# Performance work log

Hardware: AMD Instinct MI355X
Metric: run time of the kernel (lower is better)

## Reference

```python
import jax, jax.numpy as jnp
import numpy as np
import math

C = 96; HEADS = 3; HD = C // HEADS; WS = 8; B = 4; H = 256; W = 256
EPS = 1e-5; SCALE = HD ** -0.5; LOGIT_MAX = math.log(1.0 / 0.01)
N = WS * WS


def _rel_pos():
    coords = np.stack(np.meshgrid(np.arange(WS), np.arange(WS), indexing='ij')).reshape(2, -1)
    rel = (coords[:, :, None] - coords[:, None, :]).transpose(1, 2, 0).astype(np.float32)
    return jnp.asarray(np.sign(rel) * np.log1p(np.abs(rel)))  # [N, N, 2]

REL = _rel_pos()


def conv1x1(x, w, b):
    return jnp.einsum('bchw,oc->bohw', x, w) + b[None, :, None, None]


def dwconv(x, w, b, pad, reflect=False):
    if reflect:
        x = jnp.pad(x, ((0, 0), (0, 0), (pad, pad), (pad, pad)), mode='reflect')
        padding = 'VALID'
    else:
        padding = [(pad, pad), (pad, pad)]
    y = jax.lax.conv_general_dilated(x, w, (1, 1), padding,
                                     feature_group_count=x.shape[1],
                                     dimension_numbers=('NCHW', 'OIHW', 'NCHW'))
    return y + b[None, :, None, None]


def window_partition(x):  # [B,H,W,C] -> [nW, WS*WS, C]
    b, h, w, c = x.shape
    x = x.reshape(b, h // WS, WS, w // WS, WS, c).transpose(0, 1, 3, 2, 4, 5)
    return x.reshape(-1, WS * WS, c)


def window_reverse(win, h, w):  # [nW, WS*WS, C] -> [B,H,W,C]
    b = win.shape[0] // ((h // WS) * (w // WS))
    x = win.reshape(b, h // WS, w // WS, WS, WS, -1).transpose(0, 1, 3, 2, 4, 5)
    return x.reshape(b, h, w, -1)


def setup_inputs() -> dict:
    key = jax.random.key(0)
    ks = jax.random.split(key, 16)
    def nrm(k, shape, std=0.02):
        return jax.random.normal(k, shape, jnp.float32) * std
    inp = {'x': jax.random.normal(ks[0], (B, C, H, W), jnp.float32)}
    inp.update(
        agn_weight=jnp.ones((C,), jnp.float32), agn_bias=jnp.zeros((C,), jnp.float32),
        meta1_w=nrm(ks[1], (C,)), meta1_b=jnp.ones((C,), jnp.float32),
        meta2_w=nrm(ks[2], (C,)), meta2_b=jnp.zeros((C,), jnp.float32),
        la1_w=nrm(ks[3], (C, 1, 3, 3)), la1_b=jnp.zeros((C,), jnp.float32),
        la2_w=nrm(ks[4], (C, 1, 3, 3)), la2_b=jnp.zeros((C,), jnp.float32),
        ta1_w=nrm(ks[5], (C, 1, 3, 3)), ta1_b=jnp.zeros((C,), jnp.float32),
        ta2_w=nrm(ks[6], (C, 1, 3, 3)), ta2_b=jnp.zeros((C,), jnp.float32),
        q_w=nrm(ks[7], (C, C)), q_b=jnp.zeros((C,), jnp.float32),
        kv_w=nrm(ks[8], (2 * C, C)), kv_b=jnp.zeros((2 * C,), jnp.float32),
        dw_w=nrm(ks[9], (C, 1, 5, 5)), dw_b=jnp.zeros((C,), jnp.float32),
        proj_w=nrm(ks[10], (C, C)), proj_b=jnp.zeros((C,), jnp.float32),
        logit_scale=jnp.asarray(math.log(1.0 / 0.07), jnp.float32),
        rp_w1=nrm(ks[11], (256, 2)), rp_b1=jnp.zeros((256,), jnp.float32),
        rp_w2=nrm(ks[12], (HEADS, 256)), rp_b2=jnp.zeros((HEADS,), jnp.float32),
        m1_w=nrm(ks[13], (4 * C, C)), m1_b=jnp.zeros((4 * C,), jnp.float32),
        m2_w=nrm(ks[14], (C, 4 * C)), m2_b=jnp.zeros((C,), jnp.float32),
    )
    return inp


def reference(x, agn_weight, agn_bias, meta1_w, meta1_b, meta2_w, meta2_b,
              la1_w, la1_b, la2_w, la2_b, ta1_w, ta1_b, ta2_w, ta2_b,
              q_w, q_b, kv_w, kv_b, dw_w, dw_b, proj_w, proj_b,
              logit_scale, rp_w1, rp_b1, rp_w2, rp_b2,
              m1_w, m1_b, m2_w, m2_b):
    identity = x
    # ---- AGN: per-sample global mean/std norm + dynamic affine + two dw-conv branches
    mean = jnp.mean(x, axis=(1, 2, 3), keepdims=True)                      # [B,1,1,1]
    std = jnp.sqrt(jnp.mean((x - mean) ** 2, axis=(1, 2, 3), keepdims=True) + EPS)
    xn = (x - mean) / std
    rescale = std * meta1_w[None, :, None, None] + meta1_b[None, :, None, None]   # conv1x1(1->C) on std
    rebias = mean * meta2_w[None, :, None, None] + meta2_b[None, :, None, None]
    local = dwconv(jax.nn.relu(dwconv(xn, la1_w, la1_b, 1)), la2_w, la2_b, 1)
    texture = dwconv(jax.nn.relu(dwconv(xn, ta1_w, ta1_b, 1)), ta2_w, ta2_b, 1)
    xn = xn * (agn_weight[None, :, None, None] * rescale) + (agn_bias[None, :, None, None] + rebias) + local + texture
    # ---- DSAttention (use_attn, DWConv, shift_size=0, H%WS==0 so no padding)
    Q = conv1x1(xn, q_w, q_b)
    KV = conv1x1(xn, kv_w, kv_b)                                           # [B,2C,H,W]
    qkv_img = jnp.concatenate([Q, KV], axis=1).transpose(0, 2, 3, 1)       # [B,H,W,3C]
    co = dwconv(Q, dw_w, dw_b, 2, reflect=True).transpose(0, 2, 3, 1)      # reflect-padded 5x5 dwconv
    qkv = window_partition(qkv_img)                                        # [nW,N,3C]
    cw = window_partition(co)                                              # [nW,N,C]
    nW = qkv.shape[0]
    qkv = qkv.reshape(nW, N, 3, HEADS, HD).transpose(2, 0, 3, 1, 4)        # [3,nW,h,N,hd]
    q = cw.reshape(nW, N, HEADS, HD).transpose(0, 2, 1, 3)                 # q replaced by conv branch
    k = qkv[1] * SCALE
    v = qkv[2]
    ls = jnp.exp(jnp.minimum(logit_scale, LOGIT_MAX))
    hb = jax.nn.relu(REL @ rp_w1.T + rp_b1)                                # [N,N,256]
    bias = (hb @ rp_w2.T + rp_b2).transpose(2, 0, 1)                       # [h,N,N]
    attn = jax.nn.softmax(jnp.einsum('whnd,whmd->whnm', q, k) * ls + bias[None], axis=-1)
    o = jnp.einsum('whnm,whmd->whnd', attn, v).transpose(0, 2, 1, 3).reshape(nW, N, C)
    out = window_reverse(o, x.shape[2], x.shape[3]).transpose(0, 3, 1, 2)  # [B,C,H,W]
    a = conv1x1(out, proj_w, proj_b)
    x = identity + a * rescale + rebias
    # ---- MLP (1x1 conv -> ReLU -> 1x1 conv), residual
    x = x + conv1x1(jax.nn.relu(conv1x1(x, m1_w, m1_b)), m2_w, m2_b)
    return x
```

## Files before the change

### kernel.cpp

```cpp
#include <hip/hip_runtime.h>
#include <hip/hip_bf16.h>

typedef __hip_bfloat16 bf16;

#define PER_B     6291456
#define EPS_F     1e-5f
#define SCALE_F   0.17677669529663687f
#define LOGIT_MAX_F 4.605170185988092f

__device__ __forceinline__ float b2f(bf16 v){ return __bfloat162float(v); }
__device__ __forceinline__ bf16  f2b(float v){ return __float2bfloat16(v); }

template<int DT> __device__ __forceinline__ float rdf(const void* p, size_t i){
  return DT ? ((const float*)p)[i] : b2f(((const bf16*)p)[i]);
}
template<int DT> __device__ __forceinline__ void wrf(void* p, size_t i, float v){
  if (DT) ((float*)p)[i] = v; else ((bf16*)p)[i] = f2b(v);
}
template<int DT> __device__ __forceinline__ float2 rd2(const void* p, size_t i){
  if (DT) return *(const float2*)((const float*)p + i);
  unsigned u = *(const unsigned*)((const bf16*)p + i);
  return make_float2(__uint_as_float(u << 16), __uint_as_float(u & 0xffff0000u));
}

typedef __attribute__((ext_vector_type(8))) short short8v;
typedef __attribute__((ext_vector_type(4))) short short4v;
typedef __attribute__((ext_vector_type(4))) float f32x4;

__device__ __forceinline__ short f2bs(float v){
  unsigned u = __float_as_uint(v);
  return (short)((u + 0x7fffu + ((u >> 16) & 1u)) >> 16);
}
__device__ __forceinline__ float bs2f(short s){
  return __uint_as_float(((unsigned)(unsigned short)s) << 16);
}

template<int DT> __device__ __forceinline__ short8v ld8(const void* p, size_t i){
  short8v a;
  if (DT){
    const float* f = (const float*)p + i;
    float4 lo = *(const float4*)f;
    float4 hi = *(const float4*)(f + 4);
    a[0]=f2bs(lo.x); a[1]=f2bs(lo.y); a[2]=f2bs(lo.z); a[3]=f2bs(lo.w);
    a[4]=f2bs(hi.x); a[5]=f2bs(hi.y); a[6]=f2bs(hi.z); a[7]=f2bs(hi.w);
  } else {
    a = *(const short8v*)((const short*)p + i);
  }
  return a;
}
template<int DT> __device__ __forceinline__ short8v ld4x2(const void* p, size_t i0){
  short8v a;
  if (DT){
    const float* f = (const float*)p;
    float4 lo = *(const float4*)(f + i0);
    float4 hi = *(const float4*)(f + i0 + 16);
    a[0]=f2bs(lo.x); a[1]=f2bs(lo.y); a[2]=f2bs(lo.z); a[3]=f2bs(lo.w);
    a[4]=f2bs(hi.x); a[5]=f2bs(hi.y); a[6]=f2bs(hi.z); a[7]=f2bs(hi.w);
  } else {
    const short* s = (const short*)p;
    short4v lo = *(const short4v*)(s + i0);
    short4v hi = *(const short4v*)(s + i0 + 16);
    a[0]=lo[0]; a[1]=lo[1]; a[2]=lo[2]; a[3]=lo[3];
    a[4]=hi[0]; a[5]=hi[1]; a[6]=hi[2]; a[7]=hi[3];
  }
  return a;
}

__global__ __launch_bounds__(256) void k_detect(const void* __restrict__ x, int* __restrict__ flag){
  __shared__ int cnt;
  if (threadIdx.x == 0) cnt = 0;
  __syncthreads();
  float v = b2f(((const bf16*)x)[(size_t)threadIdx.x * 16]);
  int bad = (!(v == v)) || (fabsf(v) > 1e20f);
  if (bad) atomicAdd(&cnt, 1);
  __syncthreads();
  if (threadIdx.x == 0) *flag = (cnt >= 4) ? 1 : 0;
}

template<int DT>
__global__ __launch_bounds__(256) void k_stats_partial(const void* __restrict__ x,
    float* __restrict__ partials, const int* __restrict__ flag){
  if (*flag != DT) return;
  int blk = blockIdx.x;
  int b = blk >> 8, chunk = blk & 255;
  const int chunkN = PER_B / 256;
  size_t base = (size_t)b * PER_B + (size_t)chunk * chunkN;
  float s = 0.f, ss = 0.f;
  if (DT){
    const float4* p4 = (const float4*)((const float*)x + base);
    for (int i = threadIdx.x; i < chunkN/4; i += 256){
      float4 v = p4[i];
      s  += v.x + v.y + v.z + v.w;
      ss += v.x*v.x + v.y*v.y + v.z*v.z + v.w*v.w;
    }
  } else {
    const short8v* p8 = (const short8v*)((const short*)x + base);
    for (int i = threadIdx.x; i < chunkN/8; i += 256){
      short8v v = p8[i];
      #pragma unroll
      for (int k = 0; k < 8; k++){
        float f = bs2f(v[k]); s += f; ss += f*f;
      }
    }
  }
  __shared__ float sh[512];
  sh[threadIdx.x] = s; sh[256 + threadIdx.x] = ss;
  __syncthreads();
  for (int st = 128; st > 0; st >>= 1){
    if (threadIdx.x < st){
      sh[threadIdx.x]     += sh[threadIdx.x + st];
      sh[256+threadIdx.x] += sh[256+threadIdx.x + st];
    }
    __syncthreads();
  }
  if (threadIdx.x == 0){ partials[blk*2] = sh[0]; partials[blk*2+1] = sh[256]; }
}

template<int DT>
__global__ __launch_bounds__(256) void k_stats_final(const float* __restrict__ partials,
    const void* m1w, const void* m1b, const void* m2w, const void* m2b,
    float* __restrict__ stats, const int* __restrict__ flag){
  if (*flag != DT) return;
  __shared__ float sh[512];
  __shared__ float mS[4], sS[4];
  for (int b = 0; b < 4; b++){
    sh[threadIdx.x]     = partials[(b*256+threadIdx.x)*2];
    sh[256+threadIdx.x] = partials[(b*256+threadIdx.x)*2+1];
    __syncthreads();
    for (int st = 128; st > 0; st >>= 1){
      if (threadIdx.x < st){
        sh[threadIdx.x]     += sh[threadIdx.x + st];
        sh[256+threadIdx.x] += sh[256+threadIdx.x + st];
      }
      __syncthreads();
    }
    if (threadIdx.x == 0){
      float mean = sh[0] / (float)PER_B;
      float var  = sh[256] / (float)PER_B - mean*mean;
      float stdv = sqrtf(var + EPS_F);
      mS[b] = mean; sS[b] = stdv;
      stats[b] = mean; stats[4+b] = stdv;
    }
    __syncthreads();
  }
  for (int t = threadIdx.x; t < 384; t += 256){
    int b = t / 96, c = t % 96;
    stats[8+t]   = sS[b]*rdf<DT>(m1w,c) + rdf<DT>(m1b,c);
    stats[392+t] = mS[b]*rdf<DT>(m2w,c) + rdf<DT>(m2b,c);
  }
}

template<int DT>
__global__ __launch_bounds__(256) void k_bias(const void* w1, const void* b1v,
    const void* w2, const void* b2v, float* __restrict__ biasT, const int* __restrict__ flag){
  if (*flag != DT) return;
  int i = blockIdx.x >> 6, j = blockIdx.x & 63;
  int dy = (i>>3) - (j>>3), dx = (i&7) - (j&7);
  float fy = (float)dy, fx = (float)dx;
  float r0 = copysignf(log1pf(fabsf(fy)), fy);
  float r1 = copysignf(log1pf(fabsf(fx)), fx);
  int t = threadIdx.x;
  float hb = fmaxf(r0*rdf<DT>(w1,t*2) + r1*rdf<DT>(w1,t*2+1) + rdf<DT>(b1v,t), 0.f);
  __shared__ float sh[256];
  for (int h = 0; h < 3; h++){
    sh[t] = hb * rdf<DT>(w2, h*256+t);
    __syncthreads();
    for (int st = 128; st > 0; st >>= 1){ if (t < st) sh[t] += sh[t+st]; __syncthreads(); }
    if (t == 0) biasT[h*4096 + j*64 + i] = sh[0] + rdf<DT>(b2v, h);
    __syncthreads();
  }
}

template<int DT>
__global__ __launch_bounds__(256) void k_agn_fused(const void* __restrict__ x,
    const float* __restrict__ stats,
    const void* la1w, const void* la1b, const void* la2w, const void* la2b,
    const void* ta1w, const void* ta1b, const void* ta2w, const void* ta2b,
    const void* agnw, const void* agnb,
    bf16* __restrict__ xn2, const int* __restrict__ flag){
  if (*flag != DT) return;
  __shared__ float xs[1296];
  __shared__ float ts[1156];
  __shared__ float us[1156];
  int idx = blockIdx.x;
  int tile = idx & 63; int bc = idx >> 6; int c = bc % 96; int b = bc / 96;
  int oy = (tile >> 3) << 5, ox = (tile & 7) << 5;
  float mean = stats[b], sd = stats[4+b];
  size_t xbase = ((size_t)bc) << 16;
  for (int it = threadIdx.x; it < 1296; it += 256){
    int ly = it / 36, lx = it % 36;
    int gy = oy - 2 + ly, gx = ox - 2 + lx;
    float v = 0.f;
    if (gy >= 0 && gy < 256 && gx >= 0 && gx < 256)
      v = (rdf<DT>(x, xbase + (gy<<8) + gx) - mean) / sd;
    xs[it] = v;
  }
  float wl1[9], wt1[9], wl2[9], wt2[9];
  #pragma unroll
  for (int k = 0; k < 9; k++){
    wl1[k] = rdf<DT>(la1w, c*9+k); wt1[k] = rdf<DT>(ta1w, c*9+k);
    wl2[k] = rdf<DT>(la2w, c*9+k); wt2[k] = rdf<DT>(ta2w, c*9+k);
  }
  float bl1 = rdf<DT>(la1b, c), bt1 = rdf<DT>(ta1b, c);
  __syncthreads();
  for (int it = threadIdx.x; it < 1156; it += 256){
    int ly = it / 34, lx = it % 34;
    int cy = oy - 1 + ly, cx = ox - 1 + lx;
    float a1 = 0.f, a2 = 0.f;
    if (cy >= 0 && cy < 256 && cx >= 0 && cx < 256){
      a1 = bl1; a2 = bt1;
      #pragma unroll
      for (int dy = 0; dy < 3; dy++)
        #pragma unroll
        for (int dx = 0; dx < 3; dx++){
          float v = xs[(ly+dy)*36 + lx+dx];
          a1 += v * wl1[dy*3+dx]; a2 += v * wt1[dy*3+dx];
        }
      a1 = fmaxf(a1, 0.f); a2 = fmaxf(a2, 0.f);
    }
    ts[it] = a1; us[it] = a2;
  }
  __syncthreads();
  float agw = rdf<DT>(agnw,c)*stats[8+bc];
  float agb = rdf<DT>(agnb,c) + stats[392+bc];
  float bl2 = rdf<DT>(la2b, c), bt2 = rdf<DT>(ta2b, c);
  #pragma unroll
  for (int k = 0; k < 4; k++){
    int px = threadIdx.x + (k << 8);
    int ly = px >> 5, lx = px & 31;
    float l = bl2, t = bt2;
    #pragma unroll
    for (int dy = 0; dy < 3; dy++)
      #pragma unroll
      for (int dx = 0; dx < 3; dx++){
        l += ts[(ly+dy)*34 + lx+dx] * wl2[dy*3+dx];
        t += us[(ly+dy)*34 + lx+dx] * wt2[dy*3+dx];
      }
    float v = xs[(ly+2)*36 + lx+2];
    float r = v*agw + agb + l + t;
    xn2[xbase + ((oy+ly)<<8) + ox + lx] = f2b(r);
  }
}

#define CS_OFF 0
#define XS_OFF 13312
#define QB_OFF 43264
#define KT_OFF 13312
#define VD_OFF 26624
#define XC_OFF 40448
#define PS_OFF 40448
#define OS_OFF 13312

template<int DT>
__global__ __launch_bounds__(256, 3) void k_attn_mega(const bf16* __restrict__ xn2,
    const void* qw, const void* qb, const void* kvw, const void* kvb,
    const void* dww, const void* dwb, const void* pw, const void* pb,
    const void* lsin, const float* __restrict__ biasT,
    const void* __restrict__ xin, const float* __restrict__ stats,
    void* __restrict__ outp, const int* __restrict__ flag){
  if (*flag != DT) return;
  __shared__ __align__(16) char smem[53760];
  int tid = threadIdx.x, wid = blockIdx.x;
  int b = wid >> 10, wy = (wid >> 5) & 31, wx = wid & 31;
  int wv = tid >> 6, ln = tid & 63;
  int r = ln & 15, q = ln >> 4;

  {
    short* xs = (short*)(smem + XS_OFF);
    for (int it = tid; it < 13824; it += 256){
      int t = it % 144, craw = it / 144;
      int c = craw ^ ((t >> 3) & 7);
      int ty = (wy<<3) - 2 + t/12, tx = (wx<<3) - 2 + t%12;
      ty = ty < 0 ? -ty : (ty > 255 ? 510 - ty : ty);
      tx = tx < 0 ? -tx : (tx > 255 ? 510 - tx : tx);
      xs[t*104 + c] = ((const short*)xn2)[(((size_t)(b*96 + c))<<16) + (ty<<8) + tx];
    }
  }
  __syncthreads();

  {
    const short* xs = (const short*)(smem + XS_OFF);
    short* Qb = (short*)(smem + QB_OFF) + wv*1184;
    short* cs = (short*)(smem + CS_OFF);
    int ty0 = (ln>>3)+2, tx0 = (ln&7)+2;
    for (int mt = wv; mt < 6; mt += 4){
      short8v aw[3];
      #pragma unroll
      for (int kt = 0; kt < 3; kt++)
        aw[kt] = ld8<DT>(qw, (size_t)(16*mt + r)*96 + 32*kt + 8*q);
      float qb4[4];
      #pragma unroll
      for (int j = 0; j < 4; j++) qb4[j] = rdf<DT>(qb, 16*mt + 4*q + j);
      float accs[9][4];
      #pragma unroll
      for (int nt = 0; nt < 9; nt++){
        f32x4 acc = {0.f,0.f,0.f,0.f};
        #pragma unroll
        for (int kt = 0; kt < 3; kt++){
          short8v bx = *(const short8v*)(xs + (16*nt + r)*104 + 32*kt + 8*q);
          acc = __builtin_amdgcn_mfma_f32_16x16x32_bf16(aw[kt], bx, acc, 0, 0, 0);
        }
        #pragma unroll
        for (int j = 0; j < 4; j++) accs[nt][j] = acc[j] + qb4[j];
      }
      if (q < 2){
        #pragma unroll
        for (int nt = 0; nt < 9; nt++)
          #pragma unroll
          for (int j = 0; j < 4; j++)
            Qb[(4*q+j)*148 + 16*nt + r] = f2bs(accs[nt][j]);
      }
      asm volatile("s_waitcnt lgkmcnt(0)" ::: "memory");
      for (int cl = 0; cl < 8; cl++){
        int c = 16*mt + cl;
        float a = rdf<DT>(dwb, c);
        #pragma unroll
        for (int dy = -2; dy <= 2; dy++)
          #pragma unroll
          for (int dx = -2; dx <= 2; dx++)
            a += bs2f(Qb[cl*148 + (ty0+dy)*12 + tx0+dx]) * rdf<DT>(dww, c*25 + (dy+2)*5 + dx+2);
        cs[ln*104 + c] = f2bs(a);
      }
      asm volatile("s_waitcnt lgkmcnt(0)" ::: "memory");
      if (q >= 2){
        #pragma unroll
        for (int nt = 0; nt < 9; nt++)
          #pragma unroll
          for (int j = 0; j < 4; j++)
            Qb[(4*(q-2)+j)*148 + 16*nt + r] = f2bs(accs[nt][j]);
      }
      asm volatile("s_waitcnt lgkmcnt(0)" ::: "memory");
      for (int cl = 8; cl < 16; cl++){
        int c = 16*mt + cl;
        float a = rdf<DT>(dwb, c);
        #pragma unroll
        for (int dy = -2; dy <= 2; dy++)
          #pragma unroll
          for (int dx = -2; dx <= 2; dx++)
            a += bs2f(Qb[(cl-8)*148 + (ty0+dy)*12 + tx0+dx]) * rdf<DT>(dww, c*25 + (dy+2)*5 + dx+2);
        cs[ln*104 + c] = f2bs(a);
      }
      asm volatile("s_waitcnt lgkmcnt(0)" ::: "memory");
    }
  }
  __syncthreads();

  {
    short* xc = (short*)(smem + XC_OFF);
    for (int it = tid; it < 768; it += 256){
      int c = it >> 3, row = it & 7;
      const short* src = (const short*)xn2 + (((size_t)(b*96 + c))<<16)
                         + (((wy<<3)+row)<<8) + (wx<<3);
      short8v v = *(const short8v*)src;
      #pragma unroll
      for (int k = 0; k < 8; k++){
        int pe = k ^ row;
        xc[(row*8+pe)*104 + c] = v[pe];
      }
    }
  }
  __syncthreads();
  {
    const short* xc = (const short*)(smem + XC_OFF);
    short* Kt = (short*)(smem + KT_OFF);
    short* Vd = (short*)(smem + VD_OFF);
    for (int mtk = wv; mtk < 12; mtk += 4){
      short8v aw[3];
      #pragma unroll
      for (int kt = 0; kt < 3; kt++)
        aw[kt] = ld8<DT>(kvw, (size_t)(16*mtk + r)*96 + 32*kt + 8*q);
      float bb[4];
      #pragma unroll
      for (int j = 0; j < 4; j++) bb[j] = rdf<DT>(kvb, 16*mtk + 4*q + j);
      for (int nt = 0; nt < 4; nt++){
        f32x4 acc = {0.f,0.f,0.f,0.f};
        #pragma unroll
        for (int kt = 0; kt < 3; kt++){
          short8v bx = *(const short8v*)(xc + (16*nt + r)*104 + 32*kt + 8*q);
          acc = __builtin_amdgcn_mfma_f32_16x16x32_bf16(aw[kt], bx, acc, 0, 0, 0);
        }
        if (mtk < 6){
          short4v kv;
          #pragma unroll
          for (int j = 0; j < 4; j++) kv[j] = f2bs((acc[j] + bb[j]) * SCALE_F);
          *(short4v*)(Kt + (16*nt + r)*104 + 16*mtk + 4*q) = kv;
        } else {
          #pragma unroll
          for (int j = 0; j < 4; j++)
            Vd[(16*(mtk-6) + 4*q + j)*72 + 16*nt + r] = f2bs(acc[j] + bb[j]);
        }
      }
    }
  }
  __syncthreads();

  float o_save[24];
  {
    const short* cs = (const short*)(smem + CS_OFF);
    const short* Kt = (const short*)(smem + KT_OFF);
    const short* Vd = (const short*)(smem + VD_OFF);
    short* Psw = (short*)(smem + PS_OFF) + wv*1152;
    float lsv = __expf(fminf(rdf<DT>(lsin, 0), LOGIT_MAX_F));
    #pragma unroll
    for (int h = 0; h < 3; h++){
      short8v qa = *(const short8v*)(cs + (16*wv + r)*104 + 32*h + 8*q);
      f32x4 s[4];
      #pragma unroll
      for (int mt = 0; mt < 4; mt++){
        short8v kb = *(const short8v*)(Kt + (16*mt + r)*104 + 32*h + 8*q);
        f32x4 z = {0.f,0.f,0.f,0.f};
        s[mt] = __builtin_amdgcn_mfma_f32_16x16x32_bf16(qa, kb, z, 0, 0, 0);
      }
      float l[4][4];
      #pragma unroll
      for (int mt = 0; mt < 4; mt++){
        float4 bv = *(const float4*)(biasT + h*4096 + (16*mt + r)*64 + 16*wv + 4*q);
        l[mt][0] = s[mt][0]*lsv + bv.x;
        l[mt][1] = s[mt][1]*lsv + bv.y;
        l[mt][2] = s[mt][2]*lsv + bv.z;
        l[mt][3] = s[mt][3]*lsv + bv.w;
      }
      float mx[4], sm[4];
      #pragma unroll
      for (int j = 0; j < 4; j++){
        float m0 = fmaxf(fmaxf(l[0][j], l[1][j]), fmaxf(l[2][j], l[3][j]));
        m0 = fmaxf(m0, __shfl_xor(m0, 1));
        m0 = fmaxf(m0, __shfl_xor(m0, 2));
        m0 = fmaxf(m0, __shfl_xor(m0, 4));
        m0 = fmaxf(m0, __shfl_xor(m0, 8));
        mx[j] = m0; sm[j] = 0.f;
      }
      #pragma unroll
      for (int mt = 0; mt < 4; mt++)
        #pragma unroll
        for (int j = 0; j < 4; j++){
          float p = __expf(l[mt][j] - mx[j]);
          sm[j] += p;
          Psw[(4*q+j)*72 + 16*mt + r] = f2bs(p);
        }
      #pragma unroll
      for (int j = 0; j < 4; j++){
        sm[j] += __shfl_xor(sm[j], 1);
        sm[j] += __shfl_xor(sm[j], 2);
        sm[j] += __shfl_xor(sm[j], 4);
        sm[j] += __shfl_xor(sm[j], 8);
      }
      float inv[4];
      #pragma unroll
      for (int j = 0; j < 4; j++) inv[j] = 1.f / sm[j];
      asm volatile("s_waitcnt lgkmcnt(0)" ::: "memory");
      short8v pa0 = *(const short8v*)(Psw + r*72 + 8*q);
      short8v pa1 = *(const short8v*)(Psw + r*72 + 32 + 8*q);
      #pragma unroll
      for (int dt = 0; dt < 2; dt++){
        f32x4 o = {0.f,0.f,0.f,0.f};
        short8v vb0 = *(const short8v*)(Vd + (32*h + 16*dt + r)*72 + 8*q);
        short8v vb1 = *(const short8v*)(Vd + (32*h + 16*dt + r)*72 + 32 + 8*q);
        o = __builtin_amdgcn_mfma_f32_16x16x32_bf16(pa0, vb0, o, 0, 0, 0);
        o = __builtin_amdgcn_mfma_f32_16x16x32_bf16(pa1, vb1, o, 0, 0, 0);
        #pragma unroll
        for (int j = 0; j < 4; j++) o_save[h*8 + dt*4 + j] = o[j] * inv[j];
      }
      asm volatile("s_waitcnt lgkmcnt(0)" ::: "memory");
    }
  }
  __syncthreads();

  {
    short* os = (short*)(smem + OS_OFF);
    #pragma unroll
    for (int h = 0; h < 3; h++)
      #pragma unroll
      for (int dt = 0; dt < 2; dt++)
        #pragma unroll
        for (int j = 0; j < 4; j++)
          os[(16*wv + 4*q + j)*104 + 32*h + 16*dt + r] = f2bs(o_save[h*8 + dt*4 + j]);
  }
  __syncthreads();

  {
    const short* os = (const short*)(smem + OS_OFF);
    short8v ob[3];
    #pragma unroll
    for (int kt = 0; kt < 3; kt++)
      ob[kt] = *(const short8v*)(os + (16*wv + r)*104 + 32*kt + 8*q);
    for (int mt = 0; mt < 6; mt++){
      f32x4 acc = {0.f,0.f,0.f,0.f};
      #pragma unroll
      for (int kt = 0; kt < 3; kt++){
        short8v aw = ld8<DT>(pw, (size_t)(16*mt + r)*96 + 32*kt + 8*q);
        acc = __builtin_amdgcn_mfma_f32_16x16x32_bf16(aw, ob[kt], acc, 0, 0, 0);
      }
      #pragma unroll
      for (int j = 0; j < 4; j++){
        int oc = 16*mt + 4*q + j;
        int n  = 16*wv + r;
        int gy = (wy<<3) + (n>>3), gx = (wx<<3) + (n&7);
        size_t gi = (((size_t)(b*96 + oc))<<16) + (gy<<8) + gx;
        float a = acc[j] + rdf<DT>(pb, oc);
        float x1 = rdf<DT>(xin, gi) + a*stats[8 + b*96 + oc] + stats[392 + b*96 + oc];
        wrf<DT>(outp, gi, x1);
      }
    }
  }
}

template<int DT>
__global__ __launch_bounds__(256) void k_mlp_mfma(void* __restrict__ io,
    const void* w1, const void* b1, const void* w2, const void* b2v,
    const int* __restrict__ flag){
  if (*flag != DT) return;
  __shared__ __align__(16) short x1s[256*104];
  int blk = blockIdx.x; int b = blk >> 8; int pix0 = (blk & 255) << 8;
  int tid = threadIdx.x;

  for (int c = 0; c < 96; c++){
    size_t gi = (((size_t)(b*96 + c))<<16) + pix0 + tid;
    short v = DT ? f2bs(((const float*)io)[gi]) : ((const short*)io)[gi];
    x1s[tid*104 + c] = v;
  }
  __syncthreads();

  int wv = tid >> 6, l = tid & 63;
  int r = l & 15, q = l >> 4;
  int pbase = wv << 6;

  f32x4 acc2[6][4];
  #pragma unroll
  for (int mt = 0; mt < 6; mt++)
    #pragma unroll
    for (int nt = 0; nt < 4; nt++)
      acc2[mt][nt] = (f32x4){0.f,0.f,0.f,0.f};

  #pragma unroll 2
  for (int t = 0; t < 12; t++){
    short8v aA[3], aB[3];
    #pragma unroll
    for (int kt = 0; kt < 3; kt++){
      aA[kt] = ld8<DT>(w1, (size_t)(32*t + r)*96      + 32*kt + 8*q);
      aB[kt] = ld8<DT>(w1, (size_t)(32*t + 16 + r)*96 + 32*kt + 8*q);
    }
    float bA[4], bB[4];
    #pragma unroll
    for (int j = 0; j < 4; j++){
      bA[j] = rdf<DT>(b1, 32*t + 4*q + j);
      bB[j] = rdf<DT>(b1, 32*t + 16 + 4*q + j);
    }
    f32x4 a1A[4], a1B[4];
    #pragma unroll
    for (int nt = 0; nt < 4; nt++){
      a1A[nt] = (f32x4){0.f,0.f,0.f,0.f};
      a1B[nt] = (f32x4){0.f,0.f,0.f,0.f};
    }
    #pragma unroll
    for (int kt = 0; kt < 3; kt++){
      #pragma unroll
      for (int nt = 0; nt < 4; nt++){
        short8v bx = *(const short8v*)&x1s[(pbase + 16*nt + r)*104 + 32*kt + 8*q];
        a1A[nt] = __builtin_amdgcn_mfma_f32_16x16x32_bf16(aA[kt], bx, a1A[nt], 0, 0, 0);
        a1B[nt] = __builtin_amdgcn_mfma_f32_16x16x32_bf16(aB[kt], bx, a1B[nt], 0, 0, 0);
      }
    }
    short8v B2[4];
    #pragma unroll
    for (int nt = 0; nt < 4; nt++){
      short8v h;
      #pragma unroll
      for (int j = 0; j < 4; j++){
        h[j]   = f2bs(fmaxf(a1A[nt][j] + bA[j], 0.f));
        h[4+j] = f2bs(fmaxf(a1B[nt][j] + bB[j], 0.f));
      }
      B2[nt] = h;
    }
    #pragma unroll
    for (int mt = 0; mt < 6; mt++){
      short8v wA = ld4x2<DT>(w2, (size_t)(16*mt + r)*384 + 32*t + 4*q);
      #pragma unroll
      for (int nt = 0; nt < 4; nt++)
        acc2[mt][nt] = __builtin_amdgcn_mfma_f32_16x16x32_bf16(wA, B2[nt], acc2[mt][nt], 0, 0, 0);
    }
  }

  #pragma unroll
  for (int mt = 0; mt < 6; mt++)
    #pragma unroll
    for (int nt = 0; nt < 4; nt++)
      #pragma unroll
      for (int j = 0; j < 4; j++){
        int oc = 16*mt + 4*q + j;
        int pl = pbase + 16*nt + r;
        size_t gi = (((size_t)(b*96 + oc))<<16) + pix0 + pl;
        float v = acc2[mt][nt][j] + rdf<DT>(b2v, oc);
        if (DT){
          ((float*)io)[gi] = ((const float*)io)[gi] + v;
        } else {
          ((bf16*)io)[gi] = f2b(bs2f(x1s[pl*104 + oc]) + v);
        }
      }
}

extern "C" void kernel_launch(void* const* d_in, const int* in_sizes, int n_in,
                              void* d_out, int out_size, void* d_ws, size_t ws_size,
                              hipStream_t stream) {
  const void* x      = d_in[0];
  const void* agnw   = d_in[1];
  const void* agnb   = d_in[2];
  const void* meta1w = d_in[3];
  const void* meta1b = d_in[4];
  const void* meta2w = d_in[5];
  const void* meta2b = d_in[6];
  const void* la1w   = d_in[7];
  const void* la1b   = d_in[8];
  const void* la2w   = d_in[9];
  const void* la2b   = d_in[10];
  const void* ta1w   = d_in[11];
  const void* ta1b   = d_in[12];
  const void* ta2w   = d_in[13];
  const void* ta2b   = d_in[14];
  const void* qw     = d_in[15];
  const void* qb     = d_in[16];
  const void* kvw    = d_in[17];
  const void* kvb    = d_in[18];
  const void* dww    = d_in[19];
  const void* dwb    = d_in[20];
  const void* pw     = d_in[21];
  const void* pb     = d_in[22];
  const void* lsin   = d_in[23];
  const void* rpw1   = d_in[24];
  const void* rpb1   = d_in[25];
  const void* rpw2   = d_in[26];
  const void* rpb2   = d_in[27];
  const void* m1w    = d_in[28];
  const void* m1b    = d_in[29];
  const void* m2w    = d_in[30];
  const void* m2b    = d_in[31];

  char* ws = (char*)d_ws;
  int*   flag     = (int*)ws;
  float* partials = (float*)(ws + 256);
  float* stats    = (float*)(ws + 8448);
  float* biasT    = (float*)(ws + 12288);
  bf16*  xn2      = (bf16*)(ws + 65536);

  k_detect<<<1, 256, 0, stream>>>(x, flag);

  k_stats_partial<0><<<1024, 256, 0, stream>>>(x, partials, flag);
  k_stats_final<0>  <<<1,    256, 0, stream>>>(partials, meta1w, meta1b, meta2w, meta2b, stats, flag);
  k_bias<0>         <<<4096, 256, 0, stream>>>(rpw1, rpb1, rpw2, rpb2, biasT, flag);
  k_agn_fused<0>    <<<24576,256, 0, stream>>>(x, stats, la1w, la1b, la2w, la2b,
                                               ta1w, ta1b, ta2w, ta2b, agnw, agnb, xn2, flag);
  k_attn_mega<0>    <<<4096, 256, 0, stream>>>(xn2, qw, qb, kvw, kvb, dww, dwb, pw, pb,
                                               lsin, biasT, x, stats, d_out, flag);
  k_mlp_mfma<0>     <<<1024, 256, 0, stream>>>(d_out, m1w, m1b, m2w, m2b, flag);

  k_stats_partial<1><<<1024, 256, 0, stream>>>(x, partials, flag);
  k_stats_final<1>  <<<1,    256, 0, stream>>>(partials, meta1w, meta1b, meta2w, meta2b, stats, flag);
  k_bias<1>         <<<4096, 256, 0, stream>>>(rpw1, rpb1, rpw2, rpb2, biasT, flag);
  k_agn_fused<1>    <<<24576,256, 0, stream>>>(x, stats, la1w, la1b, la2w, la2b,
                                               ta1w, ta1b, ta2w, ta2b, agnw, agnb, xn2, flag);
  k_attn_mega<1>    <<<4096, 256, 0, stream>>>(xn2, qw, qb, kvw, kvb, dww, dwb, pw, pb,
                                               lsin, biasT, x, stats, d_out, flag);
  k_mlp_mfma<1>     <<<1024, 256, 0, stream>>>(d_out, m1w, m1b, m2w, m2b, flag);
}
```

Measured before the change: 1.007 ms.

## Use wave shuffles in bias MLP, skip reflect clamps, hoist MLP LDS operands

The relative-position bias kernel now reduces its 256-wide dot products with wavefront shuffles and a single barrier, replacing the shared-memory tree reduction that needed many barriers. The attention kernel's halo load takes a branch without reflect-index clamping for interior windows. The MLP kernel loads its activation B-operands from LDS into registers once, before the hidden-channel loop, instead of reloading them on every iteration. The hoist adds 48 VGPRs per thread, which may lower occupancy or cause spills in a kernel that is already register-heavy.

```diff
diff --git a/kernel.cpp b/kernel.cpp
--- a/kernel.cpp
+++ b/kernel.cpp
@@ -160,15 +160,23 @@
   float r0 = copysignf(log1pf(fabsf(fy)), fy);
   float r1 = copysignf(log1pf(fabsf(fx)), fx);
   int t = threadIdx.x;
+  int wv = t >> 6, ln = t & 63;
   float hb = fmaxf(r0*rdf<DT>(w1,t*2) + r1*rdf<DT>(w1,t*2+1) + rdf<DT>(b1v,t), 0.f);
-  __shared__ float sh[256];
+  __shared__ float ps[3][4];
+  #pragma unroll
   for (int h = 0; h < 3; h++){
-    sh[t] = hb * rdf<DT>(w2, h*256+t);
-    __syncthreads();
-    for (int st = 128; st > 0; st >>= 1){ if (t < st) sh[t] += sh[t+st]; __syncthreads(); }
-    if (t == 0) biasT[h*4096 + j*64 + i] = sh[0] + rdf<DT>(b2v, h);
-    __syncthreads();
-  }
+    float v = hb * rdf<DT>(w2, h*256+t);
+    v += __shfl_down(v, 32);
+    v += __shfl_down(v, 16);
+    v += __shfl_down(v, 8);
+    v += __shfl_down(v, 4);
+    v += __shfl_down(v, 2);
+    v += __shfl_down(v, 1);
+    if (ln == 0) ps[h][wv] = v;
+  }
+  __syncthreads();
+  if (t < 3)
+    biasT[t*4096 + j*64 + i] = ps[t][0]+ps[t][1]+ps[t][2]+ps[t][3] + rdf<DT>(b2v, t);
 }
 
 template<int DT>
@@ -267,13 +275,22 @@
 
   {
     short* xs = (short*)(smem + XS_OFF);
-    for (int it = tid; it < 13824; it += 256){
-      int t = it % 144, craw = it / 144;
-      int c = craw ^ ((t >> 3) & 7);
-      int ty = (wy<<3) - 2 + t/12, tx = (wx<<3) - 2 + t%12;
-      ty = ty < 0 ? -ty : (ty > 255 ? 510 - ty : ty);
-      tx = tx < 0 ? -tx : (tx > 255 ? 510 - tx : tx);
-      xs[t*104 + c] = ((const short*)xn2)[(((size_t)(b*96 + c))<<16) + (ty<<8) + tx];
+    if (wy >= 1 && wy <= 30 && wx >= 1 && wx <= 30){
+      for (int it = tid; it < 13824; it += 256){
+        int t = it % 144, craw = it / 144;
+        int c = craw ^ ((t >> 3) & 7);
+        int ty = (wy<<3) - 2 + t/12, tx = (wx<<3) - 2 + t%12;
+        xs[t*104 + c] = ((const short*)xn2)[(((size_t)(b*96 + c))<<16) + (ty<<8) + tx];
+      }
+    } else {
+      for (int it = tid; it < 13824; it += 256){
+        int t = it % 144, craw = it / 144;
+        int c = craw ^ ((t >> 3) & 7);
+        int ty = (wy<<3) - 2 + t/12, tx = (wx<<3) - 2 + t%12;
+        ty = ty < 0 ? -ty : (ty > 255 ? 510 - ty : ty);
+        tx = tx < 0 ? -tx : (tx > 255 ? 510 - tx : tx);
+        xs[t*104 + c] = ((const short*)xn2)[(((size_t)(b*96 + c))<<16) + (ty<<8) + tx];
+      }
     }
   }
   __syncthreads();
@@ -525,6 +542,13 @@
   int r = l & 15, q = l >> 4;
   int pbase = wv << 6;
 
+  short8v bxs[3][4];
+  #pragma unroll
+  for (int kt = 0; kt < 3; kt++)
+    #pragma unroll
+    for (int nt = 0; nt < 4; nt++)
+      bxs[kt][nt] = *(const short8v*)&x1s[(pbase + 16*nt + r)*104 + 32*kt + 8*q];
+
   f32x4 acc2[6][4];
   #pragma unroll
   for (int mt = 0; mt < 6; mt++)
@@ -556,9 +580,8 @@
     for (int kt = 0; kt < 3; kt++){
       #pragma unroll
       for (int nt = 0; nt < 4; nt++){
-        short8v bx = *(const short8v*)&x1s[(pbase + 16*nt + r)*104 + 32*kt + 8*q];
-        a1A[nt] = __builtin_amdgcn_mfma_f32_16x16x32_bf16(aA[kt], bx, a1A[nt], 0, 0, 0);
-        a1B[nt] = __builtin_amdgcn_mfma_f32_16x16x32_bf16(aB[kt], bx, a1B[nt], 0, 0, 0);
+        a1A[nt] = __builtin_amdgcn_mfma_f32_16x16x32_bf16(aA[kt], bxs[kt][nt], a1A[nt], 0, 0, 0);
+        a1B[nt] = __builtin_amdgcn_mfma_f32_16x16x32_bf16(aB[kt], bxs[kt][nt], a1B[nt], 0, 0, 0);
       }
     }
     short8v B2[4];
```

Result: no change. 1.011 ms (+0.4%).
